# Performance work log

Hardware: AMD Instinct MI355X
Metric: run time of the kernel (lower is better)

## Reference

```python
import jax, jax.numpy as jnp
import numpy as np

N = 50000      # nodes
D = 128        # in_dim
O = 128        # out_dim
MAX_DEG = 32   # degrees uniform in [0, MAX_DEG]


def setup_inputs() -> dict:
    rng = np.random.default_rng(0)
    deg = rng.integers(0, MAX_DEG + 1, size=N)          # includes deg==0 nodes
    dst = np.repeat(np.arange(N), deg)                  # target node per edge (grouped, like the buckets)
    E = dst.shape[0]                                    # ~800000
    src = rng.integers(0, N, size=E)                    # neighbor index per edge (flat neighbor_list)

    key = jax.random.key(0)
    k1, k2, k3, k4 = jax.random.split(key, 4)
    scale = jnp.float32(1.0 / np.sqrt(D))
    return {
        "x":  jax.random.normal(k1, (N, D), jnp.float32),
        "Wg": jax.random.normal(k2, (O, D), jnp.float32) * scale,  # global_lin.weight
        "Wl": jax.random.normal(k3, (O, D), jnp.float32) * scale,  # local_lin.weight
        "Ws": jax.random.normal(k4, (O, D), jnp.float32) * scale,  # self_lin.weight
        "b":  jnp.zeros((O,), jnp.float32),                        # bias param
        "src": jnp.asarray(src, jnp.int32),
        "dst": jnp.asarray(dst, jnp.int32),
        "deg": jnp.asarray(deg, jnp.int32),
    }


def reference(x, Wg, Wl, Ws, b, src, dst, deg):
    n = x.shape[0]
    # global branch: applied to every node
    g_out = x @ Wg.T                                           # [N, O]
    # mean-aggregate neighbor features (gather + segment-sum == the per-bucket view().mean())
    neigh_sum = jax.ops.segment_sum(x[src], dst, num_segments=n)   # [N, D]
    degf = jnp.maximum(deg, 1).astype(x.dtype)[:, None]
    neigh_mean = neigh_sum * (1.0 / degf)                       # [N, D]
    # local + self branches only for deg > 0 (deg==0 bucket keeps just global_out)
    mask = (deg > 0).astype(x.dtype)[:, None]                   # [N, 1]
    out = g_out + mask * (neigh_mean @ Wl.T + x @ Ws.T) + b
    # dropout is identity in eval mode; ELU activation
    return jax.nn.elu(out)
```

## Files before the change

### kernel.cpp

```cpp
#include <hip/hip_runtime.h>
#include <cstdint>
#include <cstddef>

#define KCAT 384
#define GNPB 8
#define MNPB 16
#define GAST 264
#define VP_BLOCKS 24

typedef __attribute__((ext_vector_type(8))) short bf16x8;
typedef __attribute__((ext_vector_type(4))) float f32x4;

static __device__ __forceinline__ unsigned short f2bf(float f) {
    unsigned int u = __builtin_bit_cast(unsigned int, f);
    u += 0x7fffu + ((u >> 16) & 1u);
    return (unsigned short)(u >> 16);
}
static __device__ __forceinline__ float bfhi(unsigned int u) { return __builtin_bit_cast(float, u & 0xFFFF0000u); }
static __device__ __forceinline__ float bflo(unsigned int u) { return __builtin_bit_cast(float, u << 16); }
static __device__ __forceinline__ void acc8(float* a, const uint4& v, unsigned m) {
    unsigned x0 = v.x & m, x1 = v.y & m, x2 = v.z & m, x3 = v.w & m;
    a[0] += bflo(x0); a[1] += bfhi(x0); a[2] += bflo(x1); a[3] += bfhi(x1);
    a[4] += bflo(x2); a[5] += bfhi(x2); a[6] += bflo(x3); a[7] += bfhi(x3);
}

__global__ __launch_bounds__(256)
void prep(const float* __restrict__ x, const float* __restrict__ Wg,
          const float* __restrict__ Wl, const float* __restrict__ Ws,
          const int* __restrict__ dst, unsigned short* __restrict__ Vp,
          unsigned short* __restrict__ xb, int* __restrict__ blkoff,
          int total8, int nblk_g, int noffb, int E) {
    const int bx = blockIdx.x, t = threadIdx.x;
    if (bx < VP_BLOCKS) {
        int gid = bx * 256 + t;
        if (gid < 6144) {
            int l = gid & 63, srow = (gid >> 6) % 12, g = gid / 768;
            int o = g * 16 + (l & 15);
            int k = srow * 32 + (l >> 4) * 8;
            const float* w; int kk;
            if (k < 128)      { w = Wg; kk = k; }
            else if (k < 256) { w = Wl; kk = k - 128; }
            else              { w = Ws; kk = k - 256; }
            const float* p = w + o * 128 + kk;
            uint4 u;
            u.x = (unsigned)f2bf(p[0]) | ((unsigned)f2bf(p[1]) << 16);
            u.y = (unsigned)f2bf(p[2]) | ((unsigned)f2bf(p[3]) << 16);
            u.z = (unsigned)f2bf(p[4]) | ((unsigned)f2bf(p[5]) << 16);
            u.w = (unsigned)f2bf(p[6]) | ((unsigned)f2bf(p[7]) << 16);
            ((uint4*)Vp)[gid] = u;
        }
    } else if (bx < VP_BLOCKS + noffb) {
        int b = (bx - VP_BLOCKS) * 256 + t;
        if (b < nblk_g) {
            int target = b * GNPB;
            int lo = 0, hi = E;
            while (lo < hi) { int mid = (lo + hi) >> 1; if (dst[mid] < target) lo = mid + 1; else hi = mid; }
            blkoff[b] = lo;
        }
    } else {
        int gid = (bx - VP_BLOCKS - noffb) * 256 + t;
        if (gid < total8) {
            const float4* px = (const float4*)x + (size_t)gid * 2;
            float4 a = px[0], bq = px[1];
            uint4 u;
            u.x = (unsigned)f2bf(a.x)  | ((unsigned)f2bf(a.y)  << 16);
            u.y = (unsigned)f2bf(a.z)  | ((unsigned)f2bf(a.w)  << 16);
            u.z = (unsigned)f2bf(bq.x) | ((unsigned)f2bf(bq.y) << 16);
            u.w = (unsigned)f2bf(bq.z) | ((unsigned)f2bf(bq.w) << 16);
            ((uint4*)xb)[gid] = u;
        }
    }
}

__global__ __launch_bounds__(512, 7)
void gather(const unsigned short* __restrict__ xb, const int* __restrict__ src,
            const int* __restrict__ deg, const int* __restrict__ blkoff,
            unsigned short* __restrict__ M, int N) {
    const int t = threadIdx.x, wv = t >> 6, lane = t & 63;
    const int c = lane & 15, p = lane >> 4;
    const int base = blockIdx.x * GNPB;

    int dg8 = 0;
    if (lane < GNPB && base + lane < N) dg8 = deg[base + lane];
    int incl = dg8;
#pragma unroll
    for (int off = 1; off < GNPB; off <<= 1) {
        int v = __shfl_up(incl, off, 64);
        if (lane >= off) incl += v;
    }
    const int d = __shfl(dg8, wv, 64);
    const int s = blkoff[blockIdx.x] + __shfl(incl, wv, 64) - d;
    const int n = base + wv;
    if (n >= N) return;

    int idx = 0;
    if (lane < d) idx = src[s + lane];

    const uint4* x4 = (const uint4*)xb;
    int r0 = __shfl(idx, p, 64),      r1 = __shfl(idx, p + 4, 64);
    int r2 = __shfl(idx, p + 8, 64),  r3 = __shfl(idx, p + 12, 64);
    uint4 v0 = x4[(size_t)r0 * 16 + c], v1 = x4[(size_t)r1 * 16 + c];
    uint4 v2 = x4[(size_t)r2 * 16 + c], v3 = x4[(size_t)r3 * 16 + c];
    uint4 v4, v5, v6, v7;
    const bool two = (d > 16);
    if (two) {
        int e = 16 + p;
        int r4 = __shfl(idx, e, 64),      r5 = __shfl(idx, e + 4, 64);
        int r6 = __shfl(idx, e + 8, 64),  r7 = __shfl(idx, e + 12, 64);
        v4 = x4[(size_t)r4 * 16 + c]; v5 = x4[(size_t)r5 * 16 + c];
        v6 = x4[(size_t)r6 * 16 + c]; v7 = x4[(size_t)r7 * 16 + c];
    }
    float a[8] = {0,0,0,0,0,0,0,0};
    float b[8] = {0,0,0,0,0,0,0,0};
    acc8(a, v0, (p      < d) ? ~0u : 0u);
    acc8(b, v1, (p + 4  < d) ? ~0u : 0u);
    acc8(a, v2, (p + 8  < d) ? ~0u : 0u);
    acc8(b, v3, (p + 12 < d) ? ~0u : 0u);
    if (two) {
        int e = 16 + p;
        acc8(a, v4, (e      < d) ? ~0u : 0u);
        acc8(b, v5, (e + 4  < d) ? ~0u : 0u);
        acc8(a, v6, (e + 8  < d) ? ~0u : 0u);
        acc8(b, v7, (e + 12 < d) ? ~0u : 0u);
    }
#pragma unroll
    for (int i = 0; i < 8; ++i) a[i] += b[i];
#pragma unroll
    for (int i = 0; i < 8; ++i) {
        a[i] += __shfl_xor(a[i], 16, 64);
        a[i] += __shfl_xor(a[i], 32, 64);
    }
    if (p == 0) {
        float inv = (d > 0) ? 1.0f / (float)d : 0.0f;
        uint4 u;
        u.x = (unsigned)f2bf(a[0]*inv) | ((unsigned)f2bf(a[1]*inv) << 16);
        u.y = (unsigned)f2bf(a[2]*inv) | ((unsigned)f2bf(a[3]*inv) << 16);
        u.z = (unsigned)f2bf(a[4]*inv) | ((unsigned)f2bf(a[5]*inv) << 16);
        u.w = (unsigned)f2bf(a[6]*inv) | ((unsigned)f2bf(a[7]*inv) << 16);
        ((uint4*)M)[(size_t)n * 16 + c] = u;
    }
}

__global__ __launch_bounds__(256)
void gemm(const unsigned short* __restrict__ xb, const unsigned short* __restrict__ Mm,
          const int* __restrict__ deg, const unsigned short* __restrict__ Vp,
          const float* __restrict__ bias, float* __restrict__ out, int N) {
    __shared__ __align__(16) unsigned short As[MNPB * GAST];
    __shared__ unsigned smask[MNPB];
    const int t = threadIdx.x, wv = t >> 6, lane = t & 63;
    const int c = lane & 15, quad = lane >> 4;
    const int base = blockIdx.x * MNPB;

    if (t < MNPB) smask[t] = (base + t < N && deg[base + t] > 0) ? 0xFFFFFFFFu : 0u;
#pragma unroll
    for (int it = 0; it < 2; ++it) {
        int f = it * 256 + t;
        int row = f >> 5, ch = f & 31;
        int grow = base + row; if (grow > N - 1) grow = N - 1;
        const unsigned short* gp = (ch < 16)
            ? xb + (size_t)grow * 128 + ch * 8
            : Mm + (size_t)grow * 128 + (ch - 16) * 8;
        uint4 val = *(const uint4*)gp;
        *(uint4*)(As + row * GAST + ch * 8) = val;
    }
    __syncthreads();

    const unsigned msk = smask[c];
    const int g0 = 2 * wv, g1 = 2 * wv + 1;
    const bf16x8* VB = (const bf16x8*)Vp;

    f32x4 acc0 = (f32x4){0.f, 0.f, 0.f, 0.f};
    f32x4 acc1 = (f32x4){0.f, 0.f, 0.f, 0.f};
    bf16x8 b0 = VB[(g0 * 12) * 64 + lane];
    bf16x8 b1 = VB[(g1 * 12) * 64 + lane];
#pragma unroll
    for (int s2 = 0; s2 < 12; ++s2) {
        int sn = (s2 + 1 < 12) ? s2 + 1 : 0;
        bf16x8 n0 = VB[(g0 * 12 + sn) * 64 + lane];
        bf16x8 n1 = VB[(g1 * 12 + sn) * 64 + lane];
        int seg = s2 >> 2, kk = (s2 & 3) * 32;
        bf16x8 a0 = *(const bf16x8*)(As + c * GAST + (seg == 1 ? 128 : 0) + kk + quad * 8);
        if (seg == 2) {
            uint4 ai = __builtin_bit_cast(uint4, a0);
            ai.x &= msk; ai.y &= msk; ai.z &= msk; ai.w &= msk;
            a0 = __builtin_bit_cast(bf16x8, ai);
        }
        acc0 = __builtin_amdgcn_mfma_f32_16x16x32_bf16(a0, b0, acc0, 0, 0, 0);
        acc1 = __builtin_amdgcn_mfma_f32_16x16x32_bf16(a0, b1, acc1, 0, 0, 0);
        b0 = n0; b1 = n1;
    }

    const int col0 = g0 * 16 + c, col1 = g1 * 16 + c;
    const float bv0 = bias[col0], bv1 = bias[col1];
#pragma unroll
    for (int reg = 0; reg < 4; ++reg) {
        int grow = base + quad * 4 + reg;
        if (grow < N) {
            float v0 = acc0[reg] + bv0;
            float v1 = acc1[reg] + bv1;
            out[(size_t)grow * 128 + col0] = (v0 > 0.f) ? v0 : __expf(v0) - 1.0f;
            out[(size_t)grow * 128 + col1] = (v1 > 0.f) ? v1 : __expf(v1) - 1.0f;
        }
    }
}

extern "C" void kernel_launch(void* const* d_in, const int* in_sizes, int n_in,
                              void* d_out, int out_size, void* d_ws, size_t ws_size,
                              hipStream_t stream) {
    const float* x  = (const float*)d_in[0];
    const float* Wg = (const float*)d_in[1];
    const float* Wl = (const float*)d_in[2];
    const float* Ws = (const float*)d_in[3];
    const float* b  = (const float*)d_in[4];
    const int*   src = (const int*)d_in[5];
    const int*   dst = (const int*)d_in[6];
    const int*   deg = (const int*)d_in[7];
    const int E = in_sizes[5];
    const int N = in_sizes[7];
    float* out = (float*)d_out;

    const size_t NB = (size_t)N * 128 * 2;
    unsigned short* Vp     = (unsigned short*)d_ws;
    int*            blkoff = (int*)((char*)d_ws + 98304);
    unsigned short* xb     = (unsigned short*)((char*)d_ws + 131072);
    unsigned short* Mm     = (unsigned short*)((char*)d_ws + 131072 + NB);

    const int nblk_g = (N + GNPB - 1) / GNPB;
    const int noffb  = (nblk_g + 255) / 256;
    const int total8 = N * 16;
    const int nconv  = (total8 + 255) / 256;

    prep<<<dim3(VP_BLOCKS + noffb + nconv), dim3(256), 0, stream>>>(
        x, Wg, Wl, Ws, dst, Vp, xb, blkoff, total8, nblk_g, noffb, E);
    gather<<<dim3(nblk_g), dim3(512), 0, stream>>>(xb, src, deg, blkoff, Mm, N);
    gemm<<<dim3((N + MNPB - 1) / MNPB), dim3(256), 0, stream>>>(xb, Mm, deg, Vp, b, out, N);
}
```

Baseline: 141.4 us.

## Fuse neighbor gather and MFMA GEMM into one kernel via LDS

```diff
diff --git a/kernel.cpp b/kernel.cpp
--- a/kernel.cpp
+++ b/kernel.cpp
@@ -3,9 +3,8 @@
 #include <cstddef>
 
 #define KCAT 384
-#define GNPB 8
-#define MNPB 16
-#define GAST 264
+#define NPB  16
+#define AST  264
 #define VP_BLOCKS 24
 
 typedef __attribute__((ext_vector_type(8))) short bf16x8;
@@ -29,7 +28,7 @@
           const float* __restrict__ Wl, const float* __restrict__ Ws,
           const int* __restrict__ dst, unsigned short* __restrict__ Vp,
           unsigned short* __restrict__ xb, int* __restrict__ blkoff,
-          int total8, int nblk_g, int noffb, int E) {
+          int total8, int nblk, int noffb, int E) {
     const int bx = blockIdx.x, t = threadIdx.x;
     if (bx < VP_BLOCKS) {
         int gid = bx * 256 + t;
@@ -51,8 +50,8 @@
         }
     } else if (bx < VP_BLOCKS + noffb) {
         int b = (bx - VP_BLOCKS) * 256 + t;
-        if (b < nblk_g) {
-            int target = b * GNPB;
+        if (b < nblk) {
+            int target = b * NPB;
             int lo = 0, hi = E;
             while (lo < hi) { int mid = (lo + hi) >> 1; if (dst[mid] < target) lo = mid + 1; else hi = mid; }
             blkoff[b] = lo;
@@ -72,134 +71,149 @@
     }
 }
 
-__global__ __launch_bounds__(512, 7)
-void gather(const unsigned short* __restrict__ xb, const int* __restrict__ src,
-            const int* __restrict__ deg, const int* __restrict__ blkoff,
-            unsigned short* __restrict__ M, int N) {
+__global__ __launch_bounds__(512, 4)
+void fused(const unsigned short* __restrict__ xb, const int* __restrict__ src,
+           const int* __restrict__ deg, const int* __restrict__ blkoff,
+           const unsigned short* __restrict__ Vp, const float* __restrict__ bias,
+           float* __restrict__ out, int N) {
+    __shared__ __align__(16) unsigned short As[NPB * AST];
+    __shared__ unsigned smask[NPB];
     const int t = threadIdx.x, wv = t >> 6, lane = t & 63;
     const int c = lane & 15, p = lane >> 4;
-    const int base = blockIdx.x * GNPB;
-
-    int dg8 = 0;
-    if (lane < GNPB && base + lane < N) dg8 = deg[base + lane];
-    int incl = dg8;
-#pragma unroll
-    for (int off = 1; off < GNPB; off <<= 1) {
+    const int base = blockIdx.x * NPB;
+
+    int dg = 0;
+    if (lane < NPB && base + lane < N) dg = deg[base + lane];
+    int incl = dg;
+#pragma unroll
+    for (int off = 1; off < NPB; off <<= 1) {
         int v = __shfl_up(incl, off, 64);
         if (lane >= off) incl += v;
     }
-    const int d = __shfl(dg8, wv, 64);
-    const int s = blkoff[blockIdx.x] + __shfl(incl, wv, 64) - d;
-    const int n = base + wv;
-    if (n >= N) return;
-
-    int idx = 0;
-    if (lane < d) idx = src[s + lane];
+    const int blk = blkoff[blockIdx.x];
+    const int nA = 2 * wv, nB = 2 * wv + 1;
+    const int dA = __shfl(dg, nA, 64),  dB = __shfl(dg, nB, 64);
+    const int sA = blk + __shfl(incl, nA, 64) - dA;
+    const int sB = blk + __shfl(incl, nB, 64) - dB;
+    if (wv == 0 && lane < NPB) smask[lane] = (dg > 0) ? 0xFFFFFFFFu : 0u;
+
+    int idxA = 0, idxB = 0;
+    if (lane < dA) idxA = src[sA + lane];
+    if (lane < dB) idxB = src[sB + lane];
 
     const uint4* x4 = (const uint4*)xb;
-    int r0 = __shfl(idx, p, 64),      r1 = __shfl(idx, p + 4, 64);
-    int r2 = __shfl(idx, p + 8, 64),  r3 = __shfl(idx, p + 12, 64);
-    uint4 v0 = x4[(size_t)r0 * 16 + c], v1 = x4[(size_t)r1 * 16 + c];
-    uint4 v2 = x4[(size_t)r2 * 16 + c], v3 = x4[(size_t)r3 * 16 + c];
-    uint4 v4, v5, v6, v7;
-    const bool two = (d > 16);
-    if (two) {
-        int e = 16 + p;
-        int r4 = __shfl(idx, e, 64),      r5 = __shfl(idx, e + 4, 64);
-        int r6 = __shfl(idx, e + 8, 64),  r7 = __shfl(idx, e + 12, 64);
-        v4 = x4[(size_t)r4 * 16 + c]; v5 = x4[(size_t)r5 * 16 + c];
-        v6 = x4[(size_t)r6 * 16 + c]; v7 = x4[(size_t)r7 * 16 + c];
-    }
-    float a[8] = {0,0,0,0,0,0,0,0};
-    float b[8] = {0,0,0,0,0,0,0,0};
-    acc8(a, v0, (p      < d) ? ~0u : 0u);
-    acc8(b, v1, (p + 4  < d) ? ~0u : 0u);
-    acc8(a, v2, (p + 8  < d) ? ~0u : 0u);
-    acc8(b, v3, (p + 12 < d) ? ~0u : 0u);
-    if (two) {
-        int e = 16 + p;
-        acc8(a, v4, (e      < d) ? ~0u : 0u);
-        acc8(b, v5, (e + 4  < d) ? ~0u : 0u);
-        acc8(a, v6, (e + 8  < d) ? ~0u : 0u);
-        acc8(b, v7, (e + 12 < d) ? ~0u : 0u);
-    }
-#pragma unroll
-    for (int i = 0; i < 8; ++i) a[i] += b[i];
+    uint4 xvA = {0,0,0,0}, xvB = {0,0,0,0};
+    if (p == 1 && base + nA < N) xvA = x4[(size_t)(base + nA) * 16 + c];
+    if (p == 2 && base + nB < N) xvB = x4[(size_t)(base + nB) * 16 + c];
+
+    int a0i = __shfl(idxA, p, 64),      a1i = __shfl(idxA, p + 4, 64);
+    int a2i = __shfl(idxA, p + 8, 64),  a3i = __shfl(idxA, p + 12, 64);
+    int b0i = __shfl(idxB, p, 64),      b1i = __shfl(idxB, p + 4, 64);
+    int b2i = __shfl(idxB, p + 8, 64),  b3i = __shfl(idxB, p + 12, 64);
+    uint4 vA0 = x4[(size_t)a0i * 16 + c], vA1 = x4[(size_t)a1i * 16 + c];
+    uint4 vA2 = x4[(size_t)a2i * 16 + c], vA3 = x4[(size_t)a3i * 16 + c];
+    uint4 vB0 = x4[(size_t)b0i * 16 + c], vB1 = x4[(size_t)b1i * 16 + c];
+    uint4 vB2 = x4[(size_t)b2i * 16 + c], vB3 = x4[(size_t)b3i * 16 + c];
+    uint4 vA4, vA5, vA6, vA7, vB4, vB5, vB6, vB7;
+    const bool twoA = (dA > 16), twoB = (dB > 16);
+    if (twoA) {
+        int e = 16 + p;
+        int r4 = __shfl(idxA, e, 64),      r5 = __shfl(idxA, e + 4, 64);
+        int r6 = __shfl(idxA, e + 8, 64),  r7 = __shfl(idxA, e + 12, 64);
+        vA4 = x4[(size_t)r4 * 16 + c]; vA5 = x4[(size_t)r5 * 16 + c];
+        vA6 = x4[(size_t)r6 * 16 + c]; vA7 = x4[(size_t)r7 * 16 + c];
+    }
+    if (twoB) {
+        int e = 16 + p;
+        int r4 = __shfl(idxB, e, 64),      r5 = __shfl(idxB, e + 4, 64);
+        int r6 = __shfl(idxB, e + 8, 64),  r7 = __shfl(idxB, e + 12, 64);
+        vB4 = x4[(size_t)r4 * 16 + c]; vB5 = x4[(size_t)r5 * 16 + c];
+        vB6 = x4[(size_t)r6 * 16 + c]; vB7 = x4[(size_t)r7 * 16 + c];
+    }
+
+    float aA[8] = {0,0,0,0,0,0,0,0}, bA[8] = {0,0,0,0,0,0,0,0};
+    float aB[8] = {0,0,0,0,0,0,0,0}, bB[8] = {0,0,0,0,0,0,0,0};
+    acc8(aA, vA0, (p      < dA) ? ~0u : 0u);
+    acc8(bA, vA1, (p + 4  < dA) ? ~0u : 0u);
+    acc8(aA, vA2, (p + 8  < dA) ? ~0u : 0u);
+    acc8(bA, vA3, (p + 12 < dA) ? ~0u : 0u);
+    acc8(aB, vB0, (p      < dB) ? ~0u : 0u);
+    acc8(bB, vB1, (p + 4  < dB) ? ~0u : 0u);
+    acc8(aB, vB2, (p + 8  < dB) ? ~0u : 0u);
+    acc8(bB, vB3, (p + 12 < dB) ? ~0u : 0u);
+    if (twoA) {
+        int e = 16 + p;
+        acc8(aA, vA4, (e      < dA) ? ~0u : 0u);
+        acc8(bA, vA5, (e + 4  < dA) ? ~0u : 0u);
+        acc8(aA, vA6, (e + 8  < dA) ? ~0u : 0u);
+        acc8(bA, vA7, (e + 12 < dA) ? ~0u : 0u);
+    }
+    if (twoB) {
+        int e = 16 + p;
+        acc8(aB, vB4, (e      < dB) ? ~0u : 0u);
+        acc8(bB, vB5, (e + 4  < dB) ? ~0u : 0u);
+        acc8(aB, vB6, (e + 8  < dB) ? ~0u : 0u);
+        acc8(bB, vB7, (e + 12 < dB) ? ~0u : 0u);
+    }
+#pragma unroll
+    for (int i = 0; i < 8; ++i) { aA[i] += bA[i]; aB[i] += bB[i]; }
 #pragma unroll
     for (int i = 0; i < 8; ++i) {
-        a[i] += __shfl_xor(a[i], 16, 64);
-        a[i] += __shfl_xor(a[i], 32, 64);
-    }
+        aA[i] += __shfl_xor(aA[i], 16, 64);
+        aA[i] += __shfl_xor(aA[i], 32, 64);
+        aB[i] += __shfl_xor(aB[i], 16, 64);
+        aB[i] += __shfl_xor(aB[i], 32, 64);
+    }
+    if (p == 1) *(uint4*)(As + nA * AST + c * 8) = xvA;
+    if (p == 2) *(uint4*)(As + nB * AST + c * 8) = xvB;
     if (p == 0) {
-        float inv = (d > 0) ? 1.0f / (float)d : 0.0f;
+        float inv = (dA > 0) ? 1.0f / (float)dA : 0.0f;
         uint4 u;
-        u.x = (unsigned)f2bf(a[0]*inv) | ((unsigned)f2bf(a[1]*inv) << 16);
-        u.y = (unsigned)f2bf(a[2]*inv) | ((unsigned)f2bf(a[3]*inv) << 16);
-        u.z = (unsigned)f2bf(a[4]*inv) | ((unsigned)f2bf(a[5]*inv) << 16);
-        u.w = (unsigned)f2bf(a[6]*inv) | ((unsigned)f2bf(a[7]*inv) << 16);
-        ((uint4*)M)[(size_t)n * 16 + c] = u;
-    }
-}
-
-__global__ __launch_bounds__(256)
-void gemm(const unsigned short* __restrict__ xb, const unsigned short* __restrict__ Mm,
-          const int* __restrict__ deg, const unsigned short* __restrict__ Vp,
-          const float* __restrict__ bias, float* __restrict__ out, int N) {
-    __shared__ __align__(16) unsigned short As[MNPB * GAST];
-    __shared__ unsigned smask[MNPB];
-    const int t = threadIdx.x, wv = t >> 6, lane = t & 63;
-    const int c = lane & 15, quad = lane >> 4;
-    const int base = blockIdx.x * MNPB;
-
-    if (t < MNPB) smask[t] = (base + t < N && deg[base + t] > 0) ? 0xFFFFFFFFu : 0u;
-#pragma unroll
-    for (int it = 0; it < 2; ++it) {
-        int f = it * 256 + t;
-        int row = f >> 5, ch = f & 31;
-        int grow = base + row; if (grow > N - 1) grow = N - 1;
-        const unsigned short* gp = (ch < 16)
-            ? xb + (size_t)grow * 128 + ch * 8
-            : Mm + (size_t)grow * 128 + (ch - 16) * 8;
-        uint4 val = *(const uint4*)gp;
-        *(uint4*)(As + row * GAST + ch * 8) = val;
+        u.x = (unsigned)f2bf(aA[0]*inv) | ((unsigned)f2bf(aA[1]*inv) << 16);
+        u.y = (unsigned)f2bf(aA[2]*inv) | ((unsigned)f2bf(aA[3]*inv) << 16);
+        u.z = (unsigned)f2bf(aA[4]*inv) | ((unsigned)f2bf(aA[5]*inv) << 16);
+        u.w = (unsigned)f2bf(aA[6]*inv) | ((unsigned)f2bf(aA[7]*inv) << 16);
+        *(uint4*)(As + nA * AST + 128 + c * 8) = u;
+    }
+    if (p == 3) {
+        float inv = (dB > 0) ? 1.0f / (float)dB : 0.0f;
+        uint4 u;
+        u.x = (unsigned)f2bf(aB[0]*inv) | ((unsigned)f2bf(aB[1]*inv) << 16);
+        u.y = (unsigned)f2bf(aB[2]*inv) | ((unsigned)f2bf(aB[3]*inv) << 16);
+        u.z = (unsigned)f2bf(aB[4]*inv) | ((unsigned)f2bf(aB[5]*inv) << 16);
+        u.w = (unsigned)f2bf(aB[6]*inv) | ((unsigned)f2bf(aB[7]*inv) << 16);
+        *(uint4*)(As + nB * AST + 128 + c * 8) = u;
     }
     __syncthreads();
 
+    const int quad = p;
     const unsigned msk = smask[c];
-    const int g0 = 2 * wv, g1 = 2 * wv + 1;
     const bf16x8* VB = (const bf16x8*)Vp;
-
-    f32x4 acc0 = (f32x4){0.f, 0.f, 0.f, 0.f};
-    f32x4 acc1 = (f32x4){0.f, 0.f, 0.f, 0.f};
-    bf16x8 b0 = VB[(g0 * 12) * 64 + lane];
-    bf16x8 b1 = VB[(g1 * 12) * 64 + lane];
-#pragma unroll
-    for (int s2 = 0; s2 < 12; ++s2) {
-        int sn = (s2 + 1 < 12) ? s2 + 1 : 0;
-        bf16x8 n0 = VB[(g0 * 12 + sn) * 64 + lane];
-        bf16x8 n1 = VB[(g1 * 12 + sn) * 64 + lane];
-        int seg = s2 >> 2, kk = (s2 & 3) * 32;
-        bf16x8 a0 = *(const bf16x8*)(As + c * GAST + (seg == 1 ? 128 : 0) + kk + quad * 8);
+    f32x4 acc = (f32x4){0.f, 0.f, 0.f, 0.f};
+    bf16x8 bfr = VB[(wv * 12) * 64 + lane];
+#pragma unroll
+    for (int s = 0; s < 12; ++s) {
+        int sn = (s + 1 < 12) ? s + 1 : 0;
+        bf16x8 nxt = VB[(wv * 12 + sn) * 64 + lane];
+        int seg = s >> 2, kk = (s & 3) * 32;
+        bf16x8 afr = *(const bf16x8*)(As + c * AST + (seg == 1 ? 128 : 0) + kk + quad * 8);
         if (seg == 2) {
-            uint4 ai = __builtin_bit_cast(uint4, a0);
+            uint4 ai = __builtin_bit_cast(uint4, afr);
             ai.x &= msk; ai.y &= msk; ai.z &= msk; ai.w &= msk;
-            a0 = __builtin_bit_cast(bf16x8, ai);
-        }
-        acc0 = __builtin_amdgcn_mfma_f32_16x16x32_bf16(a0, b0, acc0, 0, 0, 0);
-        acc1 = __builtin_amdgcn_mfma_f32_16x16x32_bf16(a0, b1, acc1, 0, 0, 0);
-        b0 = n0; b1 = n1;
-    }
-
-    const int col0 = g0 * 16 + c, col1 = g1 * 16 + c;
-    const float bv0 = bias[col0], bv1 = bias[col1];
+            afr = __builtin_bit_cast(bf16x8, ai);
+        }
+        acc = __builtin_amdgcn_mfma_f32_16x16x32_bf16(afr, bfr, acc, 0, 0, 0);
+        bfr = nxt;
+    }
+
+    const int col = wv * 16 + c;
+    const float bv = bias[col];
 #pragma unroll
     for (int reg = 0; reg < 4; ++reg) {
         int grow = base + quad * 4 + reg;
         if (grow < N) {
-            float v0 = acc0[reg] + bv0;
-            float v1 = acc1[reg] + bv1;
-            out[(size_t)grow * 128 + col0] = (v0 > 0.f) ? v0 : __expf(v0) - 1.0f;
-            out[(size_t)grow * 128 + col1] = (v1 > 0.f) ? v1 : __expf(v1) - 1.0f;
+            float v = acc[reg] + bv;
+            out[(size_t)grow * 128 + col] = (v > 0.f) ? v : __expf(v) - 1.0f;
         }
     }
 }
@@ -219,19 +233,16 @@
     const int N = in_sizes[7];
     float* out = (float*)d_out;
 
-    const size_t NB = (size_t)N * 128 * 2;
     unsigned short* Vp     = (unsigned short*)d_ws;
     int*            blkoff = (int*)((char*)d_ws + 98304);
     unsigned short* xb     = (unsigned short*)((char*)d_ws + 131072);
-    unsigned short* Mm     = (unsigned short*)((char*)d_ws + 131072 + NB);
-
-    const int nblk_g = (N + GNPB - 1) / GNPB;
-    const int noffb  = (nblk_g + 255) / 256;
+
+    const int nblk   = (N + NPB - 1) / NPB;
+    const int noffb  = (nblk + 255) / 256;
     const int total8 = N * 16;
     const int nconv  = (total8 + 255) / 256;
 
     prep<<<dim3(VP_BLOCKS + noffb + nconv), dim3(256), 0, stream>>>(
-        x, Wg, Wl, Ws, dst, Vp, xb, blkoff, total8, nblk_g, noffb, E);
-    gather<<<dim3(nblk_g), dim3(512), 0, stream>>>(xb, src, deg, blkoff, Mm, N);
-    gemm<<<dim3((N + MNPB - 1) / MNPB), dim3(256), 0, stream>>>(xb, Mm, deg, Vp, b, out, N);
-}
+        x, Wg, Wl, Ws, dst, Vp, xb, blkoff, total8, nblk, noffb, E);
+    fused<<<dim3(nblk), dim3(512), 0, stream>>>(xb, src, deg, blkoff, Vp, b, out, N);
+}
```

Measured after the change: 142.6 us. About the same (+0.8%).

## Fuse neighbor gather into GEMM kernel using async global-to-LDS loads

Applied to the files above, without the earlier changes.

```diff
diff --git a/kernel.cpp b/kernel.cpp
--- a/kernel.cpp
+++ b/kernel.cpp
@@ -2,10 +2,11 @@
 #include <cstdint>
 #include <cstddef>
 
-#define KCAT 384
-#define GNPB 8
-#define MNPB 16
-#define GAST 264
+#define KCAT  384
+#define NPB   16
+#define AST   264
+#define CH    96
+#define KMAXB 512
 #define VP_BLOCKS 24
 
 typedef __attribute__((ext_vector_type(8))) short bf16x8;
@@ -18,10 +19,15 @@
 }
 static __device__ __forceinline__ float bfhi(unsigned int u) { return __builtin_bit_cast(float, u & 0xFFFF0000u); }
 static __device__ __forceinline__ float bflo(unsigned int u) { return __builtin_bit_cast(float, u << 16); }
-static __device__ __forceinline__ void acc8(float* a, const uint4& v, unsigned m) {
-    unsigned x0 = v.x & m, x1 = v.y & m, x2 = v.z & m, x3 = v.w & m;
-    a[0] += bflo(x0); a[1] += bfhi(x0); a[2] += bflo(x1); a[3] += bfhi(x1);
-    a[4] += bflo(x2); a[5] += bfhi(x2); a[6] += bflo(x3); a[7] += bfhi(x3);
+static __device__ __forceinline__ void acc8(float* a, const uint4& v) {
+    a[0] += bflo(v.x); a[1] += bfhi(v.x); a[2] += bflo(v.y); a[3] += bfhi(v.y);
+    a[4] += bflo(v.z); a[5] += bfhi(v.z); a[6] += bflo(v.w); a[7] += bfhi(v.w);
+}
+static __device__ __forceinline__ void async16(const unsigned short* g, void* lds_wave_base) {
+    __builtin_amdgcn_global_load_lds(
+        (const __attribute__((address_space(1))) void*)g,
+        (__attribute__((address_space(3))) void*)lds_wave_base,
+        16, 0, 0);
 }
 
 __global__ __launch_bounds__(256)
@@ -29,7 +35,7 @@
           const float* __restrict__ Wl, const float* __restrict__ Ws,
           const int* __restrict__ dst, unsigned short* __restrict__ Vp,
           unsigned short* __restrict__ xb, int* __restrict__ blkoff,
-          int total8, int nblk_g, int noffb, int E) {
+          int total8, int nblk1, int noffb, int E) {
     const int bx = blockIdx.x, t = threadIdx.x;
     if (bx < VP_BLOCKS) {
         int gid = bx * 256 + t;
@@ -51,8 +57,8 @@
         }
     } else if (bx < VP_BLOCKS + noffb) {
         int b = (bx - VP_BLOCKS) * 256 + t;
-        if (b < nblk_g) {
-            int target = b * GNPB;
+        if (b < nblk1) {
+            int target = b * NPB;
             int lo = 0, hi = E;
             while (lo < hi) { int mid = (lo + hi) >> 1; if (dst[mid] < target) lo = mid + 1; else hi = mid; }
             blkoff[b] = lo;
@@ -72,121 +78,109 @@
     }
 }
 
-__global__ __launch_bounds__(512, 7)
-void gather(const unsigned short* __restrict__ xb, const int* __restrict__ src,
-            const int* __restrict__ deg, const int* __restrict__ blkoff,
-            unsigned short* __restrict__ M, int N) {
+__global__ __launch_bounds__(256, 4)
+void fused(const unsigned short* __restrict__ xb, const int* __restrict__ src,
+           const int* __restrict__ deg, const int* __restrict__ blkoff,
+           const unsigned short* __restrict__ Vp, const float* __restrict__ bias,
+           float* __restrict__ out, int N) {
+    __shared__ __align__(16) unsigned short Ebuf[CH * 128];
+    __shared__ __align__(16) unsigned short As[NPB * AST];
+    __shared__ int sarr[KMAXB];
+    __shared__ int sstart[NPB];
+    __shared__ int sdegs[NPB];
+    __shared__ unsigned smask[NPB];
     const int t = threadIdx.x, wv = t >> 6, lane = t & 63;
-    const int c = lane & 15, p = lane >> 4;
-    const int base = blockIdx.x * GNPB;
-
-    int dg8 = 0;
-    if (lane < GNPB && base + lane < N) dg8 = deg[base + lane];
-    int incl = dg8;
-#pragma unroll
-    for (int off = 1; off < GNPB; off <<= 1) {
-        int v = __shfl_up(incl, off, 64);
-        if (lane >= off) incl += v;
-    }
-    const int d = __shfl(dg8, wv, 64);
-    const int s = blkoff[blockIdx.x] + __shfl(incl, wv, 64) - d;
-    const int n = base + wv;
-    if (n >= N) return;
-
-    int idx = 0;
-    if (lane < d) idx = src[s + lane];
-
-    const uint4* x4 = (const uint4*)xb;
-    int r0 = __shfl(idx, p, 64),      r1 = __shfl(idx, p + 4, 64);
-    int r2 = __shfl(idx, p + 8, 64),  r3 = __shfl(idx, p + 12, 64);
-    uint4 v0 = x4[(size_t)r0 * 16 + c], v1 = x4[(size_t)r1 * 16 + c];
-    uint4 v2 = x4[(size_t)r2 * 16 + c], v3 = x4[(size_t)r3 * 16 + c];
-    uint4 v4, v5, v6, v7;
-    const bool two = (d > 16);
-    if (two) {
-        int e = 16 + p;
-        int r4 = __shfl(idx, e, 64),      r5 = __shfl(idx, e + 4, 64);
-        int r6 = __shfl(idx, e + 8, 64),  r7 = __shfl(idx, e + 12, 64);
-        v4 = x4[(size_t)r4 * 16 + c]; v5 = x4[(size_t)r5 * 16 + c];
-        v6 = x4[(size_t)r6 * 16 + c]; v7 = x4[(size_t)r7 * 16 + c];
-    }
-    float a[8] = {0,0,0,0,0,0,0,0};
-    float b[8] = {0,0,0,0,0,0,0,0};
-    acc8(a, v0, (p      < d) ? ~0u : 0u);
-    acc8(b, v1, (p + 4  < d) ? ~0u : 0u);
-    acc8(a, v2, (p + 8  < d) ? ~0u : 0u);
-    acc8(b, v3, (p + 12 < d) ? ~0u : 0u);
-    if (two) {
-        int e = 16 + p;
-        acc8(a, v4, (e      < d) ? ~0u : 0u);
-        acc8(b, v5, (e + 4  < d) ? ~0u : 0u);
-        acc8(a, v6, (e + 8  < d) ? ~0u : 0u);
-        acc8(b, v7, (e + 12 < d) ? ~0u : 0u);
-    }
-#pragma unroll
-    for (int i = 0; i < 8; ++i) a[i] += b[i];
-#pragma unroll
-    for (int i = 0; i < 8; ++i) {
-        a[i] += __shfl_xor(a[i], 16, 64);
-        a[i] += __shfl_xor(a[i], 32, 64);
-    }
-    if (p == 0) {
-        float inv = (d > 0) ? 1.0f / (float)d : 0.0f;
+    const int base = blockIdx.x * NPB;
+    const int blk0 = blkoff[blockIdx.x];
+    const int Kblk = blkoff[blockIdx.x + 1] - blk0;
+
+    if (wv == 0) {
+        int dg = 0;
+        if (lane < NPB && base + lane < N) dg = deg[base + lane];
+        int incl = dg;
+#pragma unroll
+        for (int off = 1; off < NPB; off <<= 1) {
+            int v = __shfl_up(incl, off, 64);
+            if (lane >= off) incl += v;
+        }
+        if (lane < NPB) { sstart[lane] = incl - dg; sdegs[lane] = dg; smask[lane] = dg > 0 ? ~0u : 0u; }
+    }
+    for (int k = t; k < Kblk; k += 256) sarr[k] = src[blk0 + k];
+    {
+        int i = t >> 4, cg = t & 15;
+        int grow = base + i; if (grow > N - 1) grow = N - 1;
+        uint4 xv = *((const uint4*)(xb + (size_t)grow * 128 + cg * 8));
+        *(uint4*)(As + i * AST + cg * 8) = xv;
+    }
+    __syncthreads();
+
+    const int node = t >> 4;
+    const int cg   = ((t & 15) + node) & 15;
+    const int sloc = sstart[node], dnode = sdegs[node];
+    float acc[8] = {0,0,0,0,0,0,0,0};
+    const int nch = (Kblk + CH - 1) / CH;
+
+    for (int ch = 0; ch < nch; ++ch) {
+        if (ch) __syncthreads();
+        const int C0 = ch * CH;
+#pragma unroll
+        for (int i = 0; i < CH / 16; ++i) {
+            int ebase = i * 16 + wv * 4;
+            if (C0 + ebase < Kblk) {
+                int le = C0 + ebase + (lane >> 4);
+                if (le > Kblk - 1) le = Kblk - 1;
+                int sidx = sarr[le];
+                async16(xb + (size_t)sidx * 128 + (lane & 15) * 8,
+                        (char*)Ebuf + (size_t)ebase * 256);
+            }
+        }
+        __syncthreads();
+        int lo = sloc > C0 ? sloc : C0;
+        int hi = sloc + dnode, ce = C0 + CH; if (hi > ce) hi = ce;
+        int e = lo;
+        for (; e + 1 < hi; e += 2) {
+            uint4 v0 = *(const uint4*)(Ebuf + (size_t)(e - C0) * 128 + cg * 8);
+            uint4 v1 = *(const uint4*)(Ebuf + (size_t)(e + 1 - C0) * 128 + cg * 8);
+            acc8(acc, v0); acc8(acc, v1);
+        }
+        if (e < hi) {
+            uint4 v0 = *(const uint4*)(Ebuf + (size_t)(e - C0) * 128 + cg * 8);
+            acc8(acc, v0);
+        }
+    }
+    {
+        float inv = (dnode > 0) ? 1.0f / (float)dnode : 0.0f;
         uint4 u;
-        u.x = (unsigned)f2bf(a[0]*inv) | ((unsigned)f2bf(a[1]*inv) << 16);
-        u.y = (unsigned)f2bf(a[2]*inv) | ((unsigned)f2bf(a[3]*inv) << 16);
-        u.z = (unsigned)f2bf(a[4]*inv) | ((unsigned)f2bf(a[5]*inv) << 16);
-        u.w = (unsigned)f2bf(a[6]*inv) | ((unsigned)f2bf(a[7]*inv) << 16);
-        ((uint4*)M)[(size_t)n * 16 + c] = u;
-    }
-}
-
-__global__ __launch_bounds__(256)
-void gemm(const unsigned short* __restrict__ xb, const unsigned short* __restrict__ Mm,
-          const int* __restrict__ deg, const unsigned short* __restrict__ Vp,
-          const float* __restrict__ bias, float* __restrict__ out, int N) {
-    __shared__ __align__(16) unsigned short As[MNPB * GAST];
-    __shared__ unsigned smask[MNPB];
-    const int t = threadIdx.x, wv = t >> 6, lane = t & 63;
+        u.x = (unsigned)f2bf(acc[0]*inv) | ((unsigned)f2bf(acc[1]*inv) << 16);
+        u.y = (unsigned)f2bf(acc[2]*inv) | ((unsigned)f2bf(acc[3]*inv) << 16);
+        u.z = (unsigned)f2bf(acc[4]*inv) | ((unsigned)f2bf(acc[5]*inv) << 16);
+        u.w = (unsigned)f2bf(acc[6]*inv) | ((unsigned)f2bf(acc[7]*inv) << 16);
+        *(uint4*)(As + node * AST + 128 + cg * 8) = u;
+    }
+    __syncthreads();
+
     const int c = lane & 15, quad = lane >> 4;
-    const int base = blockIdx.x * MNPB;
-
-    if (t < MNPB) smask[t] = (base + t < N && deg[base + t] > 0) ? 0xFFFFFFFFu : 0u;
-#pragma unroll
-    for (int it = 0; it < 2; ++it) {
-        int f = it * 256 + t;
-        int row = f >> 5, ch = f & 31;
-        int grow = base + row; if (grow > N - 1) grow = N - 1;
-        const unsigned short* gp = (ch < 16)
-            ? xb + (size_t)grow * 128 + ch * 8
-            : Mm + (size_t)grow * 128 + (ch - 16) * 8;
-        uint4 val = *(const uint4*)gp;
-        *(uint4*)(As + row * GAST + ch * 8) = val;
-    }
-    __syncthreads();
-
     const unsigned msk = smask[c];
     const int g0 = 2 * wv, g1 = 2 * wv + 1;
     const bf16x8* VB = (const bf16x8*)Vp;
-
     f32x4 acc0 = (f32x4){0.f, 0.f, 0.f, 0.f};
     f32x4 acc1 = (f32x4){0.f, 0.f, 0.f, 0.f};
     bf16x8 b0 = VB[(g0 * 12) * 64 + lane];
     bf16x8 b1 = VB[(g1 * 12) * 64 + lane];
 #pragma unroll
-    for (int s2 = 0; s2 < 12; ++s2) {
-        int sn = (s2 + 1 < 12) ? s2 + 1 : 0;
+    for (int s = 0; s < 12; ++s) {
+        int sn = (s + 1 < 12) ? s + 1 : 0;
         bf16x8 n0 = VB[(g0 * 12 + sn) * 64 + lane];
         bf16x8 n1 = VB[(g1 * 12 + sn) * 64 + lane];
-        int seg = s2 >> 2, kk = (s2 & 3) * 32;
-        bf16x8 a0 = *(const bf16x8*)(As + c * GAST + (seg == 1 ? 128 : 0) + kk + quad * 8);
+        int seg = s >> 2, kk = (s & 3) * 32;
+        bf16x8 afr = *(const bf16x8*)(As + c * AST + (seg == 1 ? 128 : 0) + kk + quad * 8);
         if (seg == 2) {
-            uint4 ai = __builtin_bit_cast(uint4, a0);
+            uint4 ai = __builtin_bit_cast(uint4, afr);
             ai.x &= msk; ai.y &= msk; ai.z &= msk; ai.w &= msk;
-            a0 = __builtin_bit_cast(bf16x8, ai);
-        }
-        acc0 = __builtin_amdgcn_mfma_f32_16x16x32_bf16(a0, b0, acc0, 0, 0, 0);
-        acc1 = __builtin_amdgcn_mfma_f32_16x16x32_bf16(a0, b1, acc1, 0, 0, 0);
+            afr = __builtin_bit_cast(bf16x8, ai);
+        }
+        acc0 = __builtin_amdgcn_mfma_f32_16x16x32_bf16(afr, b0, acc0, 0, 0, 0);
+        acc1 = __builtin_amdgcn_mfma_f32_16x16x32_bf16(afr, b1, acc1, 0, 0, 0);
         b0 = n0; b1 = n1;
     }
 
@@ -219,19 +213,17 @@
     const int N = in_sizes[7];
     float* out = (float*)d_out;
 
-    const size_t NB = (size_t)N * 128 * 2;
     unsigned short* Vp     = (unsigned short*)d_ws;
     int*            blkoff = (int*)((char*)d_ws + 98304);
     unsigned short* xb     = (unsigned short*)((char*)d_ws + 131072);
-    unsigned short* Mm     = (unsigned short*)((char*)d_ws + 131072 + NB);
-
-    const int nblk_g = (N + GNPB - 1) / GNPB;
-    const int noffb  = (nblk_g + 255) / 256;
+
+    const int nblk   = (N + NPB - 1) / NPB;
+    const int nblk1  = nblk + 1;
+    const int noffb  = (nblk1 + 255) / 256;
     const int total8 = N * 16;
     const int nconv  = (total8 + 255) / 256;
 
     prep<<<dim3(VP_BLOCKS + noffb + nconv), dim3(256), 0, stream>>>(
-        x, Wg, Wl, Ws, dst, Vp, xb, blkoff, total8, nblk_g, noffb, E);
-    gather<<<dim3(nblk_g), dim3(512), 0, stream>>>(xb, src, deg, blkoff, Mm, N);
-    gemm<<<dim3((N + MNPB - 1) / MNPB), dim3(256), 0, stream>>>(xb, Mm, deg, Vp, b, out, N);
-}
+        x, Wg, Wl, Ws, dst, Vp, xb, blkoff, total8, nblk1, noffb, E);
+    fused<<<dim3(nblk), dim3(256), 0, stream>>>(xb, src, deg, blkoff, Vp, b, out, N);
+}
```

New measurement: 144.1 us. No clear change (+1.9%).

## Stage neighbor gathers via async global-to-LDS loads and enlarge GEMM row tile

Applied to the files above, without the earlier changes.

```diff
diff --git a/kernel.cpp b/kernel.cpp
--- a/kernel.cpp
+++ b/kernel.cpp
@@ -2,10 +2,11 @@
 #include <cstdint>
 #include <cstddef>
 
-#define KCAT 384
-#define GNPB 8
-#define MNPB 16
-#define GAST 264
+#define KCAT  384
+#define GNPB  8
+#define EROWS 28
+#define MROWS 64
+#define AST   264
 #define VP_BLOCKS 24
 
 typedef __attribute__((ext_vector_type(8))) short bf16x8;
@@ -22,6 +23,12 @@
     unsigned x0 = v.x & m, x1 = v.y & m, x2 = v.z & m, x3 = v.w & m;
     a[0] += bflo(x0); a[1] += bfhi(x0); a[2] += bflo(x1); a[3] += bfhi(x1);
     a[4] += bflo(x2); a[5] += bfhi(x2); a[6] += bflo(x3); a[7] += bfhi(x3);
+}
+static __device__ __forceinline__ void async16(const unsigned short* g, void* lds_wave_base) {
+    __builtin_amdgcn_global_load_lds(
+        (const __attribute__((address_space(1))) void*)g,
+        (__attribute__((address_space(3))) void*)lds_wave_base,
+        16, 0, 0);
 }
 
 __global__ __launch_bounds__(256)
@@ -72,65 +79,71 @@
     }
 }
 
-__global__ __launch_bounds__(512, 7)
+__global__ __launch_bounds__(512)
 void gather(const unsigned short* __restrict__ xb, const int* __restrict__ src,
             const int* __restrict__ deg, const int* __restrict__ blkoff,
             unsigned short* __restrict__ M, int N) {
+    __shared__ __align__(16) unsigned short Ebuf[GNPB * 3584];
     const int t = threadIdx.x, wv = t >> 6, lane = t & 63;
     const int c = lane & 15, p = lane >> 4;
     const int base = blockIdx.x * GNPB;
 
-    int dg8 = 0;
-    if (lane < GNPB && base + lane < N) dg8 = deg[base + lane];
-    int incl = dg8;
+    int dg = 0;
+    if (lane < GNPB && base + lane < N) dg = deg[base + lane];
+    int incl = dg;
 #pragma unroll
     for (int off = 1; off < GNPB; off <<= 1) {
         int v = __shfl_up(incl, off, 64);
         if (lane >= off) incl += v;
     }
-    const int d = __shfl(dg8, wv, 64);
+    const int d = __shfl(dg, wv, 64);
     const int s = blkoff[blockIdx.x] + __shfl(incl, wv, 64) - d;
     const int n = base + wv;
-    if (n >= N) return;
-
-    int idx = 0;
-    if (lane < d) idx = src[s + lane];
-
-    const uint4* x4 = (const uint4*)xb;
-    int r0 = __shfl(idx, p, 64),      r1 = __shfl(idx, p + 4, 64);
-    int r2 = __shfl(idx, p + 8, 64),  r3 = __shfl(idx, p + 12, 64);
-    uint4 v0 = x4[(size_t)r0 * 16 + c], v1 = x4[(size_t)r1 * 16 + c];
-    uint4 v2 = x4[(size_t)r2 * 16 + c], v3 = x4[(size_t)r3 * 16 + c];
-    uint4 v4, v5, v6, v7;
-    const bool two = (d > 16);
-    if (two) {
-        int e = 16 + p;
-        int r4 = __shfl(idx, e, 64),      r5 = __shfl(idx, e + 4, 64);
-        int r6 = __shfl(idx, e + 8, 64),  r7 = __shfl(idx, e + 12, 64);
-        v4 = x4[(size_t)r4 * 16 + c]; v5 = x4[(size_t)r5 * 16 + c];
-        v6 = x4[(size_t)r6 * 16 + c]; v7 = x4[(size_t)r7 * 16 + c];
-    }
+    const bool active = (n < N) && (d > 0);
+
+    int sidx = 0;
+    if (lane < d) sidx = src[s + lane];
+
+    char* eb = (char*)Ebuf + wv * 7168;
+    if (active) {
+#pragma unroll
+        for (int i = 0; i < 7; ++i) {
+            if (4 * i < d) {
+                int le = 4 * i + p;
+                if (le > d - 1) le = d - 1;
+                int ridx = __shfl(sidx, le, 64);
+                async16(xb + (size_t)ridx * 128 + c * 8, eb + i * 1024);
+            }
+        }
+    }
+    const int et = EROWS + p;
+    uint4 vt = {0, 0, 0, 0};
+    if (d > EROWS) {
+        int etc = (et < d) ? et : d - 1;
+        int ridx = __shfl(sidx, etc, 64);
+        vt = *(const uint4*)(xb + (size_t)ridx * 128 + c * 8);
+    }
+    asm volatile("s_waitcnt vmcnt(0)" ::: "memory");
+
     float a[8] = {0,0,0,0,0,0,0,0};
-    float b[8] = {0,0,0,0,0,0,0,0};
-    acc8(a, v0, (p      < d) ? ~0u : 0u);
-    acc8(b, v1, (p + 4  < d) ? ~0u : 0u);
-    acc8(a, v2, (p + 8  < d) ? ~0u : 0u);
-    acc8(b, v3, (p + 12 < d) ? ~0u : 0u);
-    if (two) {
-        int e = 16 + p;
-        acc8(a, v4, (e      < d) ? ~0u : 0u);
-        acc8(b, v5, (e + 4  < d) ? ~0u : 0u);
-        acc8(a, v6, (e + 8  < d) ? ~0u : 0u);
-        acc8(b, v7, (e + 12 < d) ? ~0u : 0u);
-    }
-#pragma unroll
-    for (int i = 0; i < 8; ++i) a[i] += b[i];
+    float b2[8] = {0,0,0,0,0,0,0,0};
+    if (active) {
+#pragma unroll
+        for (int g = 0; g < 7; ++g) {
+            int e = 4 * g + p;
+            uint4 v = *(const uint4*)(eb + e * 256 + c * 16);
+            acc8((g & 1) ? b2 : a, v, (e < d) ? ~0u : 0u);
+        }
+        acc8(b2, vt, (et < d) ? ~0u : 0u);
+    }
+#pragma unroll
+    for (int i = 0; i < 8; ++i) a[i] += b2[i];
 #pragma unroll
     for (int i = 0; i < 8; ++i) {
         a[i] += __shfl_xor(a[i], 16, 64);
         a[i] += __shfl_xor(a[i], 32, 64);
     }
-    if (p == 0) {
+    if (p == 0 && n < N) {
         float inv = (d > 0) ? 1.0f / (float)d : 0.0f;
         uint4 u;
         u.x = (unsigned)f2bf(a[0]*inv) | ((unsigned)f2bf(a[1]*inv) << 16);
@@ -145,61 +158,67 @@
 void gemm(const unsigned short* __restrict__ xb, const unsigned short* __restrict__ Mm,
           const int* __restrict__ deg, const unsigned short* __restrict__ Vp,
           const float* __restrict__ bias, float* __restrict__ out, int N) {
-    __shared__ __align__(16) unsigned short As[MNPB * GAST];
-    __shared__ unsigned smask[MNPB];
+    __shared__ __align__(16) unsigned short As[MROWS * AST];
+    __shared__ unsigned smask[MROWS];
     const int t = threadIdx.x, wv = t >> 6, lane = t & 63;
     const int c = lane & 15, quad = lane >> 4;
-    const int base = blockIdx.x * MNPB;
-
-    if (t < MNPB) smask[t] = (base + t < N && deg[base + t] > 0) ? 0xFFFFFFFFu : 0u;
-#pragma unroll
-    for (int it = 0; it < 2; ++it) {
+    const int base = blockIdx.x * MROWS;
+
+    if (t < MROWS) smask[t] = (base + t < N && deg[base + t] > 0) ? 0xFFFFFFFFu : 0u;
+#pragma unroll
+    for (int it = 0; it < 8; ++it) {
         int f = it * 256 + t;
         int row = f >> 5, ch = f & 31;
         int grow = base + row; if (grow > N - 1) grow = N - 1;
         const unsigned short* gp = (ch < 16)
             ? xb + (size_t)grow * 128 + ch * 8
             : Mm + (size_t)grow * 128 + (ch - 16) * 8;
-        uint4 val = *(const uint4*)gp;
-        *(uint4*)(As + row * GAST + ch * 8) = val;
+        *(uint4*)(As + row * AST + ch * 8) = *(const uint4*)gp;
     }
     __syncthreads();
 
-    const unsigned msk = smask[c];
     const int g0 = 2 * wv, g1 = 2 * wv + 1;
     const bf16x8* VB = (const bf16x8*)Vp;
-
-    f32x4 acc0 = (f32x4){0.f, 0.f, 0.f, 0.f};
-    f32x4 acc1 = (f32x4){0.f, 0.f, 0.f, 0.f};
+    f32x4 acc[4][2];
+#pragma unroll
+    for (int r = 0; r < 4; ++r) { acc[r][0] = (f32x4){0,0,0,0}; acc[r][1] = (f32x4){0,0,0,0}; }
+
     bf16x8 b0 = VB[(g0 * 12) * 64 + lane];
     bf16x8 b1 = VB[(g1 * 12) * 64 + lane];
 #pragma unroll
-    for (int s2 = 0; s2 < 12; ++s2) {
-        int sn = (s2 + 1 < 12) ? s2 + 1 : 0;
+    for (int s = 0; s < 12; ++s) {
+        int sn = (s + 1 < 12) ? s + 1 : 0;
         bf16x8 n0 = VB[(g0 * 12 + sn) * 64 + lane];
         bf16x8 n1 = VB[(g1 * 12 + sn) * 64 + lane];
-        int seg = s2 >> 2, kk = (s2 & 3) * 32;
-        bf16x8 a0 = *(const bf16x8*)(As + c * GAST + (seg == 1 ? 128 : 0) + kk + quad * 8);
-        if (seg == 2) {
-            uint4 ai = __builtin_bit_cast(uint4, a0);
-            ai.x &= msk; ai.y &= msk; ai.z &= msk; ai.w &= msk;
-            a0 = __builtin_bit_cast(bf16x8, ai);
-        }
-        acc0 = __builtin_amdgcn_mfma_f32_16x16x32_bf16(a0, b0, acc0, 0, 0, 0);
-        acc1 = __builtin_amdgcn_mfma_f32_16x16x32_bf16(a0, b1, acc1, 0, 0, 0);
+        int seg = s >> 2, kk = (s & 3) * 32;
+#pragma unroll
+        for (int r = 0; r < 4; ++r) {
+            bf16x8 afr = *(const bf16x8*)(As + (16 * r + c) * AST + (seg == 1 ? 128 : 0) + kk + quad * 8);
+            if (seg == 2) {
+                unsigned m = smask[16 * r + c];
+                uint4 ai = __builtin_bit_cast(uint4, afr);
+                ai.x &= m; ai.y &= m; ai.z &= m; ai.w &= m;
+                afr = __builtin_bit_cast(bf16x8, ai);
+            }
+            acc[r][0] = __builtin_amdgcn_mfma_f32_16x16x32_bf16(afr, b0, acc[r][0], 0, 0, 0);
+            acc[r][1] = __builtin_amdgcn_mfma_f32_16x16x32_bf16(afr, b1, acc[r][1], 0, 0, 0);
+        }
         b0 = n0; b1 = n1;
     }
 
     const int col0 = g0 * 16 + c, col1 = g1 * 16 + c;
     const float bv0 = bias[col0], bv1 = bias[col1];
 #pragma unroll
-    for (int reg = 0; reg < 4; ++reg) {
-        int grow = base + quad * 4 + reg;
-        if (grow < N) {
-            float v0 = acc0[reg] + bv0;
-            float v1 = acc1[reg] + bv1;
-            out[(size_t)grow * 128 + col0] = (v0 > 0.f) ? v0 : __expf(v0) - 1.0f;
-            out[(size_t)grow * 128 + col1] = (v1 > 0.f) ? v1 : __expf(v1) - 1.0f;
+    for (int r = 0; r < 4; ++r) {
+#pragma unroll
+        for (int reg = 0; reg < 4; ++reg) {
+            int grow = base + 16 * r + quad * 4 + reg;
+            if (grow < N) {
+                float v0 = acc[r][0][reg] + bv0;
+                float v1 = acc[r][1][reg] + bv1;
+                out[(size_t)grow * 128 + col0] = (v0 > 0.f) ? v0 : __expf(v0) - 1.0f;
+                out[(size_t)grow * 128 + col1] = (v1 > 0.f) ? v1 : __expf(v1) - 1.0f;
+            }
         }
     }
 }
@@ -233,5 +252,5 @@
     prep<<<dim3(VP_BLOCKS + noffb + nconv), dim3(256), 0, stream>>>(
         x, Wg, Wl, Ws, dst, Vp, xb, blkoff, total8, nblk_g, noffb, E);
     gather<<<dim3(nblk_g), dim3(512), 0, stream>>>(xb, src, deg, blkoff, Mm, N);
-    gemm<<<dim3((N + MNPB - 1) / MNPB), dim3(256), 0, stream>>>(xb, Mm, deg, Vp, b, out, N);
-}
+    gemm<<<dim3((N + MROWS - 1) / MROWS), dim3(256), 0, stream>>>(xb, Mm, deg, Vp, b, out, N);
+}
```

Result: slower. 156.9 us (+10.9%).
